# Optimization experiments

Hardware: AMD Instinct MI355X
Metric: run time of the kernel (lower is better)

The kernel has to match this reference:

```python
import jax, jax.numpy as jnp
import numpy as np

VOCAB, TAGS, EMB, HID = 50257, 64, 512, 1024
B, S = 64, 512
H = HID // 2  # per-direction LSTM hidden size
NEG = -10000.0


def _lstm_dir(xs, w_ih, w_hh, b_ih, b_hh):
    # xs: (S, B, E) time-major. PyTorch gate order: i, f, g, o.
    pre = jnp.einsum('sbe,ge->sbg', xs, w_ih) + b_ih + b_hh  # (S, B, 4H)
    Bq = xs.shape[1]
    Hq = w_hh.shape[1]

    def step(carry, x_pre):
        h, c = carry
        g = x_pre + h @ w_hh.T
        i, f, gg, o = jnp.split(g, 4, axis=-1)
        c = jax.nn.sigmoid(f) * c + jax.nn.sigmoid(i) * jnp.tanh(gg)
        h = jax.nn.sigmoid(o) * jnp.tanh(c)
        return (h, c), h

    init = (jnp.zeros((Bq, Hq), xs.dtype), jnp.zeros((Bq, Hq), xs.dtype))
    _, hs = jax.lax.scan(step, init, pre)
    return hs  # (S, B, H)


def _crf_forward(emissions, transitions):
    # emissions: (B, S, T); returns log partition per batch element
    Bq, Sq, T = emissions.shape
    alpha0 = jnp.full((Bq, T), NEG, emissions.dtype).at[:, 0].set(0.0)

    def step(alpha, emit):
        # alpha: (B, T_prev); emit: (B, T_next)
        a = alpha[:, None, :] + transitions[None, :, :] + emit[:, :, None]
        return jax.scipy.special.logsumexp(a, axis=2), None

    alpha, _ = jax.lax.scan(step, alpha0, jnp.swapaxes(emissions, 0, 1))
    return jax.scipy.special.logsumexp(alpha, axis=1)


def _gold_score(emissions, tags, transitions):
    Bq = emissions.shape[0]
    tags_ext = jnp.concatenate(
        [jnp.zeros((Bq, 1), dtype=tags.dtype), tags], axis=1)  # (B, S+1)
    emit = jnp.take_along_axis(emissions, tags[:, :, None], axis=2)
    emit = emit[..., 0].sum(axis=1)  # (B,)
    trans = transitions[tags_ext[:, 1:], tags_ext[:, :-1]].sum(axis=1)  # (B,)
    return emit + trans


def setup_inputs() -> dict:
    key = jax.random.key(0)
    ks = jax.random.split(key, 16)
    sentences = jax.random.randint(ks[0], (B, S), 0, VOCAB)
    tags = jax.random.randint(ks[1], (B, S), 0, TAGS)
    lengths = jnp.full((B,), S, dtype=jnp.int32)

    sc = 1.0 / np.sqrt(H)
    u = lambda k, shp: jax.random.uniform(k, shp, jnp.float32, -sc, sc)
    emb = jax.random.normal(ks[2], (VOCAB, EMB), jnp.float32)
    emb = emb.at[0].set(0.0)  # padding_idx=0
    w_ih_f, w_hh_f = u(ks[3], (4 * H, EMB)), u(ks[4], (4 * H, H))
    b_ih_f, b_hh_f = u(ks[5], (4 * H,)), u(ks[6], (4 * H,))
    w_ih_b, w_hh_b = u(ks[7], (4 * H, EMB)), u(ks[8], (4 * H, H))
    b_ih_b, b_hh_b = u(ks[9], (4 * H,)), u(ks[10], (4 * H,))
    w_out = u(ks[11], (TAGS, HID))
    b_out = u(ks[12], (TAGS,))
    transitions = jax.random.normal(ks[13], (TAGS, TAGS), jnp.float32)
    transitions = transitions.at[:, 0].set(NEG).at[0, :].set(NEG)
    return dict(sentences=sentences, tags=tags, lengths=lengths, emb=emb,
                w_ih_f=w_ih_f, w_hh_f=w_hh_f, b_ih_f=b_ih_f, b_hh_f=b_hh_f,
                w_ih_b=w_ih_b, w_hh_b=w_hh_b, b_ih_b=b_ih_b, b_hh_b=b_hh_b,
                w_out=w_out, b_out=b_out, transitions=transitions)


def reference(sentences, tags, lengths, emb, w_ih_f, w_hh_f, b_ih_f, b_hh_f,
              w_ih_b, w_hh_b, b_ih_b, b_hh_b, w_out, b_out, transitions):
    x = emb[sentences]                       # (B, S, E)
    xs = jnp.swapaxes(x, 0, 1)               # (S, B, E) time-major
    h_f = _lstm_dir(xs, w_ih_f, w_hh_f, b_ih_f, b_hh_f)           # (S, B, H)
    h_b = _lstm_dir(xs[::-1], w_ih_b, w_hh_b, b_ih_b, b_hh_b)[::-1]
    lstm_out = jnp.concatenate([h_f, h_b], axis=-1)               # (S, B, 2H)
    lstm_out = jnp.swapaxes(lstm_out, 0, 1)                       # (B, S, 2H)
    emissions = lstm_out @ w_out.T + b_out                        # (B, S, T)
    gold = _gold_score(emissions, tags, transitions)
    fwd = _crf_forward(emissions, transitions)
    return jnp.mean(fwd - gold)
```

## Files before the change

### kernel.cpp

```cpp
#include <hip/hip_runtime.h>

#define NB 64
#define NS 512
#define NE 512
#define NH 512
#define NG 2048
#define NT 64
#define KC 1024
#define HB 16777216
#define SENT32 0x7FC07FC0u
#define NEGV (-10000.0f)

typedef __attribute__((ext_vector_type(8))) short bf16x8;
typedef __attribute__((ext_vector_type(4))) float f32x4;
typedef unsigned short u16;
typedef unsigned int u32;
typedef unsigned long long u64;

__device__ __forceinline__ u16 f2bf(float x) {
    unsigned u = __builtin_bit_cast(unsigned, x);
    u += 0x7fffu + ((u >> 16) & 1u);
    return (u16)(u >> 16);
}
__device__ __forceinline__ float sig_(float x) {
    return __builtin_amdgcn_rcpf(1.0f + __builtin_amdgcn_exp2f(-1.44269504f * x));
}
__device__ __forceinline__ float tanh_(float x) {
    return 2.0f * __builtin_amdgcn_rcpf(1.0f + __builtin_amdgcn_exp2f(-2.88539009f * x)) - 1.0f;
}

__global__ void prep_wcomb(const float* __restrict__ wihf, const float* __restrict__ whhf,
                           const float* __restrict__ wihb, const float* __restrict__ whhb,
                           u16* __restrict__ wcomb) {
    int idx = blockIdx.x * 256 + threadIdx.x;
    int base = idx * 4;
    int d = base >> 21;
    int rem = base & ((1 << 21) - 1);
    int n = rem >> 10;
    int k = rem & 1023;
    const float* wih = d ? wihb : wihf;
    const float* whh = d ? whhb : whhf;
    const float* src = (k < NE) ? (wih + n * NE + k) : (whh + n * NH + (k - NE));
    float4 v = *reinterpret_cast<const float4*>(src);
    ushort4 o;
    o.x = f2bf(v.x); o.y = f2bf(v.y); o.z = f2bf(v.z); o.w = f2bf(v.w);
    *reinterpret_cast<ushort4*>(wcomb + base) = o;
}

__global__ void prep_misc(const float* __restrict__ wout,
                          const float* __restrict__ bihf, const float* __restrict__ bhhf,
                          const float* __restrict__ bihb, const float* __restrict__ bhhb,
                          u16* __restrict__ woutbf, float* __restrict__ bias) {
    int idx = blockIdx.x * 256 + threadIdx.x;
    if (idx < 65536) { woutbf[idx] = f2bf(wout[idx]); return; }
    idx -= 65536;
    if (idx < 4096) {
        int d = idx >> 11, g = idx & 2047;
        bias[idx] = d ? (bihb[g] + bhhb[g]) : (bihf[g] + bhhf[g]);
    }
}

__global__ void prep_hfill(uint4* __restrict__ h) {
    int idx = blockIdx.x * 256 + threadIdx.x;
    uint4 v = {SENT32, SENT32, SENT32, SENT32};
    h[idx] = v;
}

__global__ void prep_embed(const float* __restrict__ emb, const int* __restrict__ sents,
                           u16* __restrict__ xbf) {
    int idx = blockIdx.x * 256 + threadIdx.x;
    int m = idx >> 7;
    int e = (idx & 127) << 2;
    int s = m >> 6, b = m & 63;
    int tok = sents[b * NS + s];
    float4 v = *reinterpret_cast<const float4*>(emb + (size_t)tok * NE + e);
    ushort4 o;
    o.x = f2bf(v.x); o.y = f2bf(v.y); o.z = f2bf(v.z); o.w = f2bf(v.w);
    *reinterpret_cast<ushort4*>(xbf + (size_t)m * NE + e) = o;
}

__global__ __launch_bounds__(512, 1)
void lstm_persist(const u16* __restrict__ xbf, const u16* __restrict__ wcomb,
                  const float* __restrict__ bias, u16* __restrict__ hall) {
    const int jblk = blockIdx.x;
    const int dir  = blockIdx.y;
    const int t = threadIdx.x;
    const int w = t >> 6, l = t & 63;
    const int l16 = l & 15, lhi = l >> 4;
    const int kbase = w * 128;
    const bool isx = (w < 4);

    __shared__ float gred[8][64][68];

    bf16x8 bfrag[4][4];
#pragma unroll
    for (int nf = 0; nf < 4; ++nf)
#pragma unroll
        for (int kt = 0; kt < 4; ++kt) {
            int gr = nf * NH + jblk * 16 + l16;
            int k = kbase + kt * 32 + lhi * 8;
            bfrag[nf][kt] = *reinterpret_cast<const bf16x8*>(
                wcomb + (size_t)(dir * NG + gr) * KC + k);
        }

    const int bb = t >> 3;
    const int jo = t & 7;
    const int j0 = jo * 2;
    float breg[4][2];
#pragma unroll
    for (int gi = 0; gi < 4; ++gi)
#pragma unroll
        for (int u = 0; u < 2; ++u)
            breg[gi][u] = bias[dir * NG + gi * NH + jblk * 16 + j0 + u];
    float c0 = 0.f, c1 = 0.f;

    u32* Hw = reinterpret_cast<u32*>(hall) + (size_t)dir * (HB / 2);
    const u64* Hq = reinterpret_cast<const u64*>(hall) + (size_t)dir * (HB / 4);

    for (int step = 0; step < NS; ++step) {
        const int s = dir ? (NS - 1 - step) : step;
        const int sprev = dir ? (s + 1) : (s - 1);

        f32x4 acc[4][4];
#pragma unroll
        for (int mf = 0; mf < 4; ++mf)
#pragma unroll
            for (int nf = 0; nf < 4; ++nf)
                acc[mf][nf] = (f32x4){0.f, 0.f, 0.f, 0.f};

        if (isx) {
            const u16* Abase = xbf + (size_t)(s * NB) * NE + kbase;
#pragma unroll
            for (int kt = 0; kt < 4; ++kt) {
                int k = kt * 32 + lhi * 8;
#pragma unroll
                for (int mf = 0; mf < 4; ++mf) {
                    bf16x8 a = *reinterpret_cast<const bf16x8*>(Abase + (size_t)(mf * 16 + l16) * NE + k);
#pragma unroll
                    for (int nf = 0; nf < 4; ++nf)
                        acc[mf][nf] = __builtin_amdgcn_mfma_f32_16x16x32_bf16(a, bfrag[nf][kt], acc[mf][nf], 0, 0, 0);
                }
            }
        } else if (step > 0) {
            const int kloc = kbase - 512;
            u64 qa[4][4], qb[4][4];
            u32 okm = 0;
#pragma unroll
            for (int kt = 0; kt < 4; ++kt) {
                int j = kloc + kt * 32 + lhi * 8;
#pragma unroll
                for (int mf = 0; mf < 4; ++mf) {
                    const u64* P = Hq + (size_t)(sprev * NB + mf * 16 + l16) * 128 + (j >> 2);
                    u64 v0 = __hip_atomic_load(P,     __ATOMIC_RELAXED, __HIP_MEMORY_SCOPE_AGENT);
                    u64 v1 = __hip_atomic_load(P + 1, __ATOMIC_RELAXED, __HIP_MEMORY_SCOPE_AGENT);
                    qa[kt][mf] = v0; qb[kt][mf] = v1;
                    bool bad = ((u32)v0 == SENT32) | ((u32)(v0 >> 32) == SENT32)
                             | ((u32)v1 == SENT32) | ((u32)(v1 >> 32) == SENT32);
                    okm |= (bad ? 0u : 1u) << (kt * 4 + mf);
                }
            }
            while (__ballot(okm != 0xFFFFu)) {
                __builtin_amdgcn_s_sleep(1);
#pragma unroll
                for (int kt = 0; kt < 4; ++kt) {
                    int j = kloc + kt * 32 + lhi * 8;
#pragma unroll
                    for (int mf = 0; mf < 4; ++mf) {
                        u32 bit = 1u << (kt * 4 + mf);
                        if (!(okm & bit)) {
                            const u64* P = Hq + (size_t)(sprev * NB + mf * 16 + l16) * 128 + (j >> 2);
                            u64 v0 = __hip_atomic_load(P,     __ATOMIC_RELAXED, __HIP_MEMORY_SCOPE_AGENT);
                            u64 v1 = __hip_atomic_load(P + 1, __ATOMIC_RELAXED, __HIP_MEMORY_SCOPE_AGENT);
                            qa[kt][mf] = v0; qb[kt][mf] = v1;
                            bool bad = ((u32)v0 == SENT32) | ((u32)(v0 >> 32) == SENT32)
                                     | ((u32)v1 == SENT32) | ((u32)(v1 >> 32) == SENT32);
                            if (!bad) okm |= bit;
                        }
                    }
                }
            }
            __builtin_amdgcn_sched_barrier(0);
#pragma unroll
            for (int kt = 0; kt < 4; ++kt) {
#pragma unroll
                for (int mf = 0; mf < 4; ++mf) {
                    union { u64 q[2]; bf16x8 v; } cv;
                    cv.q[0] = qa[kt][mf]; cv.q[1] = qb[kt][mf];
#pragma unroll
                    for (int nf = 0; nf < 4; ++nf)
                        acc[mf][nf] = __builtin_amdgcn_mfma_f32_16x16x32_bf16(cv.v, bfrag[nf][kt], acc[mf][nf], 0, 0, 0);
                }
            }
        }

#pragma unroll
        for (int mf = 0; mf < 4; ++mf)
#pragma unroll
            for (int nf = 0; nf < 4; ++nf)
#pragma unroll
                for (int r = 0; r < 4; ++r)
                    gred[w][mf * 16 + lhi * 4 + r][nf * 16 + l16] = acc[mf][nf][r];
        __syncthreads();

        float g[2][4];
#pragma unroll
        for (int u = 0; u < 2; ++u)
#pragma unroll
            for (int gi = 0; gi < 4; ++gi) {
                int n = gi * 16 + j0 + u;
                float sum = gred[0][bb][n];
#pragma unroll
                for (int kw = 1; kw < 8; ++kw) sum += gred[kw][bb][n];
                g[u][gi] = sum + breg[gi][u];
            }
        float cn0 = sig_(g[0][1]) * c0 + sig_(g[0][0]) * tanh_(g[0][2]);
        float cn1 = sig_(g[1][1]) * c1 + sig_(g[1][0]) * tanh_(g[1][2]);
        c0 = cn0; c1 = cn1;
        u32 hw = (u32)f2bf(sig_(g[0][3]) * tanh_(cn0))
               | ((u32)f2bf(sig_(g[1][3]) * tanh_(cn1)) << 16);
        __hip_atomic_store(Hw + (size_t)(s * NB + bb) * 256 + jblk * 8 + jo, hw,
                           __ATOMIC_RELAXED, __HIP_MEMORY_SCOPE_AGENT);
        __syncthreads();
    }
}

__global__ void emis_kernel(const u16* __restrict__ hall, const u16* __restrict__ woutbf,
                            const float* __restrict__ bout, float* __restrict__ emis) {
    const int blk = blockIdx.x;
    const int t = threadIdx.x;
    const int w = t >> 6, l = t & 63;
    const int l16 = l & 15, lhi = l >> 4;

    const u16* arow0 = hall + (size_t)(blk * 64 + w * 16 + l16) * NH;
    const u16* arow1 = arow0 + HB;
    const u16* br0 = woutbf + (size_t)(0 * 16 + l16) * KC;
    const u16* br1 = woutbf + (size_t)(1 * 16 + l16) * KC;
    const u16* br2 = woutbf + (size_t)(2 * 16 + l16) * KC;
    const u16* br3 = woutbf + (size_t)(3 * 16 + l16) * KC;

    f32x4 a0 = {0.f,0.f,0.f,0.f}, a1 = {0.f,0.f,0.f,0.f}, a2 = {0.f,0.f,0.f,0.f}, a3 = {0.f,0.f,0.f,0.f};
#pragma unroll
    for (int kt = 0; kt < 16; ++kt) {
        int k = kt * 32 + lhi * 8;
        bf16x8 a = *reinterpret_cast<const bf16x8*>(arow0 + k);
        a0 = __builtin_amdgcn_mfma_f32_16x16x32_bf16(a, *reinterpret_cast<const bf16x8*>(br0 + k), a0, 0, 0, 0);
        a1 = __builtin_amdgcn_mfma_f32_16x16x32_bf16(a, *reinterpret_cast<const bf16x8*>(br1 + k), a1, 0, 0, 0);
        a2 = __builtin_amdgcn_mfma_f32_16x16x32_bf16(a, *reinterpret_cast<const bf16x8*>(br2 + k), a2, 0, 0, 0);
        a3 = __builtin_amdgcn_mfma_f32_16x16x32_bf16(a, *reinterpret_cast<const bf16x8*>(br3 + k), a3, 0, 0, 0);
    }
#pragma unroll
    for (int kt = 0; kt < 16; ++kt) {
        int k = kt * 32 + lhi * 8;
        bf16x8 a = *reinterpret_cast<const bf16x8*>(arow1 + k);
        a0 = __builtin_amdgcn_mfma_f32_16x16x32_bf16(a, *reinterpret_cast<const bf16x8*>(br0 + NH + k), a0, 0, 0, 0);
        a1 = __builtin_amdgcn_mfma_f32_16x16x32_bf16(a, *reinterpret_cast<const bf16x8*>(br1 + NH + k), a1, 0, 0, 0);
        a2 = __builtin_amdgcn_mfma_f32_16x16x32_bf16(a, *reinterpret_cast<const bf16x8*>(br2 + NH + k), a2, 0, 0, 0);
        a3 = __builtin_amdgcn_mfma_f32_16x16x32_bf16(a, *reinterpret_cast<const bf16x8*>(br3 + NH + k), a3, 0, 0, 0);
    }
#pragma unroll
    for (int r = 0; r < 4; ++r) {
        int gm = blk * 64 + w * 16 + lhi * 4 + r;
        emis[(size_t)gm * NT + 0 * 16 + l16] = a0[r] + bout[0 * 16 + l16];
        emis[(size_t)gm * NT + 1 * 16 + l16] = a1[r] + bout[1 * 16 + l16];
        emis[(size_t)gm * NT + 2 * 16 + l16] = a2[r] + bout[2 * 16 + l16];
        emis[(size_t)gm * NT + 3 * 16 + l16] = a3[r] + bout[3 * 16 + l16];
    }
}

__global__ void gold_kernel(const float* __restrict__ emis, const int* __restrict__ tags,
                            const float* __restrict__ trans, float* __restrict__ gold) {
    int b = blockIdx.x, t = threadIdx.x;
    float acc = 0.f;
    for (int s = t; s < NS; s += 256) {
        int tag = tags[b * NS + s];
        int prev = (s == 0) ? 0 : tags[b * NS + s - 1];
        acc += emis[(size_t)(s * NB + b) * NT + tag] + trans[tag * NT + prev];
    }
    acc += __shfl_xor(acc, 1);  acc += __shfl_xor(acc, 2);  acc += __shfl_xor(acc, 4);
    acc += __shfl_xor(acc, 8);  acc += __shfl_xor(acc, 16); acc += __shfl_xor(acc, 32);
    __shared__ float red[4];
    if ((t & 63) == 0) red[t >> 6] = acc;
    __syncthreads();
    if (t == 0) gold[b] = red[0] + red[1] + red[2] + red[3];
}

__global__ void crf_kernel(const float* __restrict__ emis, const float* __restrict__ trans,
                           float* __restrict__ fwd) {
    int b = blockIdx.x, t = threadIdx.x;
    __shared__ float transT[64][65];
    __shared__ float alA[64], alB[64];
    for (int idx = t; idx < 4096; idx += 256) {
        int next = idx & 63, prev = idx >> 6;
        transT[prev][next] = trans[next * NT + prev];
    }
    if (t < 64) alA[t] = (t == 0) ? 0.f : NEGV;
    __syncthreads();

    int next = t >> 2, q = t & 3;
    float* cur = alA;
    float* nxt = alB;
    for (int s = 0; s < NS; ++s) {
        float emit = emis[(size_t)(s * NB + b) * NT + next];
        int p0 = q * 16;
        float M = -3.0e38f;
#pragma unroll
        for (int i = 0; i < 16; ++i) {
            float v = cur[p0 + i] + transT[p0 + i][next];
            M = fmaxf(M, v);
        }
        M = fmaxf(M, __shfl_xor(M, 1));
        M = fmaxf(M, __shfl_xor(M, 2));
        float Ssum = 0.f;
#pragma unroll
        for (int i = 0; i < 16; ++i) {
            float v = cur[p0 + i] + transT[p0 + i][next];
            Ssum += expf(v - M);
        }
        Ssum += __shfl_xor(Ssum, 1);
        Ssum += __shfl_xor(Ssum, 2);
        if (q == 0) nxt[next] = M + logf(Ssum) + emit;
        __syncthreads();
        float* tmp = cur; cur = nxt; nxt = tmp;
    }
    if (t < 64) {
        float v = cur[t];
        float M = v;
        for (int d = 1; d < 64; d <<= 1) M = fmaxf(M, __shfl_xor(M, d));
        float e = expf(v - M);
        for (int d = 1; d < 64; d <<= 1) e += __shfl_xor(e, d);
        if (t == 0) fwd[b] = M + logf(e);
    }
}

__global__ void final_kernel(const float* __restrict__ fwd, const float* __restrict__ gold,
                             float* __restrict__ out) {
    int t = threadIdx.x;
    float v = fwd[t] - gold[t];
    for (int d = 1; d < 64; d <<= 1) v += __shfl_xor(v, d);
    if (t == 0) out[0] = v * (1.0f / 64.0f);
}

extern "C" void kernel_launch(void* const* d_in, const int* in_sizes, int n_in,
                              void* d_out, int out_size, void* d_ws, size_t ws_size,
                              hipStream_t stream) {
    (void)in_sizes; (void)n_in; (void)out_size; (void)ws_size;
    const int* sents = (const int*)d_in[0];
    const int* tags  = (const int*)d_in[1];
    const float* emb  = (const float*)d_in[3];
    const float* wihf = (const float*)d_in[4];
    const float* whhf = (const float*)d_in[5];
    const float* bihf = (const float*)d_in[6];
    const float* bhhf = (const float*)d_in[7];
    const float* wihb = (const float*)d_in[8];
    const float* whhb = (const float*)d_in[9];
    const float* bihb = (const float*)d_in[10];
    const float* bhhb = (const float*)d_in[11];
    const float* wout = (const float*)d_in[12];
    const float* bout = (const float*)d_in[13];
    const float* trans = (const float*)d_in[14];

    char* ws = (char*)d_ws;
    u16*   WCOMB  = (u16*)(ws + 0);
    u16*   WOUTBF = (u16*)(ws + 8388608);
    float* BIAS   = (float*)(ws + 8519680);
    u16*   XBF    = (u16*)(ws + 8536064);
    u16*   HALL   = (u16*)(ws + 42090496);
    float* EMIS   = (float*)(ws + 109199360);
    float* FWD    = (float*)(ws + 117587968);
    float* GOLD   = (float*)(ws + 117588224);

    prep_wcomb<<<4096, 256, 0, stream>>>(wihf, whhf, wihb, whhb, WCOMB);
    prep_misc<<<272, 256, 0, stream>>>(wout, bihf, bhhf, bihb, bhhb, WOUTBF, BIAS);
    prep_hfill<<<16384, 256, 0, stream>>>((uint4*)HALL);
    prep_embed<<<16384, 256, 0, stream>>>(emb, sents, XBF);

    lstm_persist<<<dim3(32, 2), 512, 0, stream>>>(XBF, WCOMB, BIAS, HALL);

    emis_kernel<<<512, 256, 0, stream>>>(HALL, WOUTBF, bout, EMIS);
    gold_kernel<<<64, 256, 0, stream>>>(EMIS, tags, trans, GOLD);
    crf_kernel<<<64, 256, 0, stream>>>(EMIS, trans, FWD);
    final_kernel<<<1, 64, 0, stream>>>(FWD, GOLD, (float*)d_out);
}
```

Measured before the change: 4.384 ms.

## Overlap next-step input projection with gate update in persistent LSTM kernel

Restructures the recurrent loop so the four input-projection waves do the gate reduction and cell update, then immediately compute the next timestep's x·W_ih MFMAs from a prefetched register buffer while the h-waves spin on the previous step's hidden state. Input rows are prefetched two steps ahead, and each thread now handles four hidden units with 64-bit stores and vectorized LDS reads. The aim is to take the input projection and global loads off the critical serial path. In exchange it adds register pressure from the prefetch buffer and ties correctness to the reordered synchronization.

```diff
diff --git a/kernel.cpp b/kernel.cpp
--- a/kernel.cpp
+++ b/kernel.cpp
@@ -103,33 +103,34 @@
                 wcomb + (size_t)(dir * NG + gr) * KC + k);
         }
 
-    const int bb = t >> 3;
-    const int jo = t & 7;
-    const int j0 = jo * 2;
-    float breg[4][2];
-#pragma unroll
-    for (int gi = 0; gi < 4; ++gi)
-#pragma unroll
-        for (int u = 0; u < 2; ++u)
-            breg[gi][u] = bias[dir * NG + gi * NH + jblk * 16 + j0 + u];
-    float c0 = 0.f, c1 = 0.f;
-
-    u32* Hw = reinterpret_cast<u32*>(hall) + (size_t)dir * (HB / 2);
-    const u64* Hq = reinterpret_cast<const u64*>(hall) + (size_t)dir * (HB / 4);
-
-    for (int step = 0; step < NS; ++step) {
-        const int s = dir ? (NS - 1 - step) : step;
-        const int sprev = dir ? (s + 1) : (s - 1);
-
-        f32x4 acc[4][4];
+    const int bb = t >> 2;
+    const int jq = t & 3;
+    const int j0 = jq * 4;
+    float breg[4][4];
+    if (isx) {
+#pragma unroll
+        for (int gi = 0; gi < 4; ++gi)
+#pragma unroll
+            for (int u = 0; u < 4; ++u)
+                breg[gi][u] = bias[dir * NG + gi * NH + jblk * 16 + j0 + u];
+    }
+    float cc[4] = {0.f, 0.f, 0.f, 0.f};
+
+    u64* HWq = reinterpret_cast<u64*>(hall) + (size_t)dir * (HB / 4);
+    const u64* Hq = HWq;
+
+    f32x4 acc[4][4];
+    bf16x8 xpre[4][4];
+
+    {
+        const int s0 = dir ? (NS - 1) : 0;
 #pragma unroll
         for (int mf = 0; mf < 4; ++mf)
 #pragma unroll
             for (int nf = 0; nf < 4; ++nf)
                 acc[mf][nf] = (f32x4){0.f, 0.f, 0.f, 0.f};
-
         if (isx) {
-            const u16* Abase = xbf + (size_t)(s * NB) * NE + kbase;
+            const u16* Abase = xbf + (size_t)(s0 * NB) * NE + kbase;
 #pragma unroll
             for (int kt = 0; kt < 4; ++kt) {
                 int k = kt * 32 + lhi * 8;
@@ -141,7 +142,78 @@
                         acc[mf][nf] = __builtin_amdgcn_mfma_f32_16x16x32_bf16(a, bfrag[nf][kt], acc[mf][nf], 0, 0, 0);
                 }
             }
-        } else if (step > 0) {
+            const int s1 = dir ? (NS - 2) : 1;
+            const u16* Pbase = xbf + (size_t)(s1 * NB) * NE + kbase;
+#pragma unroll
+            for (int kt = 0; kt < 4; ++kt)
+#pragma unroll
+                for (int mf = 0; mf < 4; ++mf)
+                    xpre[kt][mf] = *reinterpret_cast<const bf16x8*>(
+                        Pbase + (size_t)(mf * 16 + l16) * NE + kt * 32 + lhi * 8);
+        }
+#pragma unroll
+        for (int mf = 0; mf < 4; ++mf)
+#pragma unroll
+            for (int nf = 0; nf < 4; ++nf)
+#pragma unroll
+                for (int r = 0; r < 4; ++r)
+                    gred[w][mf * 16 + lhi * 4 + r][nf * 16 + l16] = acc[mf][nf][r];
+        __syncthreads();
+    }
+
+    for (int it = 0; it < NS; ++it) {
+        const int s = dir ? (NS - 1 - it) : it;
+        const bool last = (it == NS - 1);
+
+        if (isx) {
+            f32x4 sums[4];
+#pragma unroll
+            for (int gi = 0; gi < 4; ++gi) {
+                f32x4 v = *reinterpret_cast<const f32x4*>(&gred[0][bb][gi * 16 + j0]);
+#pragma unroll
+                for (int w2 = 1; w2 < 8; ++w2)
+                    v += *reinterpret_cast<const f32x4*>(&gred[w2][bb][gi * 16 + j0]);
+                sums[gi] = v;
+            }
+            u64 hw = 0;
+#pragma unroll
+            for (int u = 0; u < 4; ++u) {
+                float gi_ = sums[0][u] + breg[0][u];
+                float gf_ = sums[1][u] + breg[1][u];
+                float gg_ = sums[2][u] + breg[2][u];
+                float go_ = sums[3][u] + breg[3][u];
+                float cn = sig_(gf_) * cc[u] + sig_(gi_) * tanh_(gg_);
+                cc[u] = cn;
+                hw |= (u64)f2bf(sig_(go_) * tanh_(cn)) << (u * 16);
+            }
+            __hip_atomic_store(HWq + (size_t)(s * NB + bb) * 128 + jblk * 4 + jq, hw,
+                               __ATOMIC_RELAXED, __HIP_MEMORY_SCOPE_AGENT);
+
+            if (!last) {
+#pragma unroll
+                for (int mf = 0; mf < 4; ++mf)
+#pragma unroll
+                    for (int nf = 0; nf < 4; ++nf)
+                        acc[mf][nf] = (f32x4){0.f, 0.f, 0.f, 0.f};
+#pragma unroll
+                for (int kt = 0; kt < 4; ++kt)
+#pragma unroll
+                    for (int mf = 0; mf < 4; ++mf)
+#pragma unroll
+                        for (int nf = 0; nf < 4; ++nf)
+                            acc[mf][nf] = __builtin_amdgcn_mfma_f32_16x16x32_bf16(xpre[kt][mf], bfrag[nf][kt], acc[mf][nf], 0, 0, 0);
+                const int s2 = dir ? (s - 2) : (s + 2);
+                if (s2 >= 0 && s2 < NS) {
+                    const u16* Pbase = xbf + (size_t)(s2 * NB) * NE + kbase;
+#pragma unroll
+                    for (int kt = 0; kt < 4; ++kt)
+#pragma unroll
+                        for (int mf = 0; mf < 4; ++mf)
+                            xpre[kt][mf] = *reinterpret_cast<const bf16x8*>(
+                                Pbase + (size_t)(mf * 16 + l16) * NE + kt * 32 + lhi * 8);
+                }
+            }
+        } else if (!last) {
             const int kloc = kbase - 512;
             u64 qa[4][4], qb[4][4];
             u32 okm = 0;
@@ -150,7 +222,7 @@
                 int j = kloc + kt * 32 + lhi * 8;
 #pragma unroll
                 for (int mf = 0; mf < 4; ++mf) {
-                    const u64* P = Hq + (size_t)(sprev * NB + mf * 16 + l16) * 128 + (j >> 2);
+                    const u64* P = Hq + (size_t)(s * NB + mf * 16 + l16) * 128 + (j >> 2);
                     u64 v0 = __hip_atomic_load(P,     __ATOMIC_RELAXED, __HIP_MEMORY_SCOPE_AGENT);
                     u64 v1 = __hip_atomic_load(P + 1, __ATOMIC_RELAXED, __HIP_MEMORY_SCOPE_AGENT);
                     qa[kt][mf] = v0; qb[kt][mf] = v1;
@@ -168,7 +240,7 @@
                     for (int mf = 0; mf < 4; ++mf) {
                         u32 bit = 1u << (kt * 4 + mf);
                         if (!(okm & bit)) {
-                            const u64* P = Hq + (size_t)(sprev * NB + mf * 16 + l16) * 128 + (j >> 2);
+                            const u64* P = Hq + (size_t)(s * NB + mf * 16 + l16) * 128 + (j >> 2);
                             u64 v0 = __hip_atomic_load(P,     __ATOMIC_RELAXED, __HIP_MEMORY_SCOPE_AGENT);
                             u64 v1 = __hip_atomic_load(P + 1, __ATOMIC_RELAXED, __HIP_MEMORY_SCOPE_AGENT);
                             qa[kt][mf] = v0; qb[kt][mf] = v1;
@@ -181,6 +253,11 @@
             }
             __builtin_amdgcn_sched_barrier(0);
 #pragma unroll
+            for (int mf = 0; mf < 4; ++mf)
+#pragma unroll
+                for (int nf = 0; nf < 4; ++nf)
+                    acc[mf][nf] = (f32x4){0.f, 0.f, 0.f, 0.f};
+#pragma unroll
             for (int kt = 0; kt < 4; ++kt) {
 #pragma unroll
                 for (int mf = 0; mf < 4; ++mf) {
@@ -193,34 +270,17 @@
             }
         }
 
-#pragma unroll
-        for (int mf = 0; mf < 4; ++mf)
-#pragma unroll
-            for (int nf = 0; nf < 4; ++nf)
-#pragma unroll
-                for (int r = 0; r < 4; ++r)
-                    gred[w][mf * 16 + lhi * 4 + r][nf * 16 + l16] = acc[mf][nf][r];
-        __syncthreads();
-
-        float g[2][4];
-#pragma unroll
-        for (int u = 0; u < 2; ++u)
-#pragma unroll
-            for (int gi = 0; gi < 4; ++gi) {
-                int n = gi * 16 + j0 + u;
-                float sum = gred[0][bb][n];
-#pragma unroll
-                for (int kw = 1; kw < 8; ++kw) sum += gred[kw][bb][n];
-                g[u][gi] = sum + breg[gi][u];
-            }
-        float cn0 = sig_(g[0][1]) * c0 + sig_(g[0][0]) * tanh_(g[0][2]);
-        float cn1 = sig_(g[1][1]) * c1 + sig_(g[1][0]) * tanh_(g[1][2]);
-        c0 = cn0; c1 = cn1;
-        u32 hw = (u32)f2bf(sig_(g[0][3]) * tanh_(cn0))
-               | ((u32)f2bf(sig_(g[1][3]) * tanh_(cn1)) << 16);
-        __hip_atomic_store(Hw + (size_t)(s * NB + bb) * 256 + jblk * 8 + jo, hw,
-                           __ATOMIC_RELAXED, __HIP_MEMORY_SCOPE_AGENT);
-        __syncthreads();
+        if (!last) {
+            __syncthreads();
+#pragma unroll
+            for (int mf = 0; mf < 4; ++mf)
+#pragma unroll
+                for (int nf = 0; nf < 4; ++nf)
+#pragma unroll
+                    for (int r = 0; r < 4; ++r)
+                        gred[w][mf * 16 + lhi * 4 + r][nf * 16 + l16] = acc[mf][nf][r];
+            __syncthreads();
+        }
     }
 }
 
```

After: 6.539 ms. 49.2% more time.
